# Kernel optimization log

Measured on AMD Instinct MI355X. Metric: run time of the kernel, lower is better.

The kernel has to match this reference:

```python
import jax, jax.numpy as jnp
import numpy as np


def setup_inputs() -> dict:
    key = jax.random.key(0)
    ks = jax.random.split(key, 7)
    B, C, H, W = 32, 512, 64, 64
    C8 = C // 8
    scale = 1.0 / np.sqrt(C)  # ~kaiming-ish for 1x1 conv
    return {
        "x": jax.random.normal(ks[0], (B, C, H, W), dtype=jnp.float32),
        "wq": jax.random.normal(ks[1], (C8, C), dtype=jnp.float32) * scale,
        "bq": jax.random.normal(ks[2], (C8,), dtype=jnp.float32) * 0.01,
        "wk": jax.random.normal(ks[3], (C8, C), dtype=jnp.float32) * scale,
        "bk": jax.random.normal(ks[4], (C8,), dtype=jnp.float32) * 0.01,
        "wv": jax.random.normal(ks[5], (C8, C), dtype=jnp.float32) * scale,
        "bv": jax.random.normal(ks[6], (C8,), dtype=jnp.float32) * 0.01,
    }


def reference(x, wq, bq, wk, bk, wv, bv):
    B, C, H, W = x.shape
    N = H * W
    xf = x.reshape(B, C, N)  # [B, C, N]
    # 1x1 convs == per-pixel linear projections C -> C//8
    q = jnp.einsum("bcn,oc->bon", xf, wq) + bq[None, :, None]  # [B, C8, N]
    k = jnp.einsum("bcn,oc->bon", xf, wk) + bk[None, :, None]  # [B, C8, N]
    v = jnp.einsum("bcn,oc->bon", xf, wv) + bv[None, :, None]  # [B, C8, N]
    # attention over channel pairs: [B, C8, C8], softmax over dim=-2 (rows)
    logits = jnp.einsum("bon,bpn->bop", q, k)
    attn = jax.nn.softmax(logits, axis=-2)
    out = jnp.einsum("bop,bpn->bon", attn, v)  # [B, C8, N]
    return out.mean(axis=-1)  # [B, C8]
```

## Files before the change

kernel.cpp:

```cpp
#include <hip/hip_runtime.h>


typedef __attribute__((ext_vector_type(8))) short short8;
typedef __attribute__((ext_vector_type(4))) float floatx4;
typedef __attribute__((ext_vector_type(4))) unsigned short ushort4v;

#define MFMA16(a, b, c) __builtin_amdgcn_mfma_f32_16x16x32_bf16((a), (b), (c), 0, 0, 0)

__device__ __forceinline__ unsigned short f2bf(float f) {
  unsigned int u = __float_as_uint(f);
  u = u + 0x7fffu + ((u >> 16) & 1u);
  return (unsigned short)(u >> 16);
}
__device__ __forceinline__ float bf2f(unsigned short h) {
  return __uint_as_float(((unsigned int)h) << 16);
}

constexpr int CB = 32;
constexpr int CC = 512;
constexpr int CO = 64;
constexpr int NN = 4096;
constexpr int NT = 128;
constexpr int KC = 32;
constexpr int NCH = CC / KC;

constexpr int XROW = 40;
constexpr int QROW = 72;

constexpr int WQH = 0;
constexpr int WQL = 2560;
constexpr int WKH = 5120;
constexpr int WKL = 7680;
constexpr int XHI = 10240;
constexpr int XLO = 15360;
constexpr int SMEM_U = 20480;
constexpr int QHI = 0, QLO = 4608, KHI = 9216, KLO = 13824;

__global__ __launch_bounds__(256, 2) void proj_kernel(
    const float* __restrict__ x, const float* __restrict__ wq,
    const float* __restrict__ bq, const float* __restrict__ wk,
    const float* __restrict__ bk, float* __restrict__ logits,
    float* __restrict__ xsum)
{
  __shared__ __align__(16) unsigned short smem[SMEM_U];

  const int t    = threadIdx.x;
  const int lane = t & 63;
  const int wave = t >> 6;
  const int quad = lane >> 4;
  const int l15  = lane & 15;
  const int b    = blockIdx.x >> 5;
  const int tile = blockIdx.x & 31;
  const int n0   = tile * NT;
  const int nlow = t & 31;
  const int chi  = t >> 5;

  floatx4 accq[4][2], acck[4][2];
#pragma unroll
  for (int mf = 0; mf < 4; ++mf)
#pragma unroll
    for (int nf = 0; nf < 2; ++nf) {
      accq[mf][nf] = (floatx4)0.0f;
      acck[mf][nf] = (floatx4)0.0f;
    }

  const float* xb = x + (size_t)b * CC * NN + n0;

  for (int ch = 0; ch < NCH; ++ch) {
    const int c0 = ch * KC;
    __syncthreads();

    float xs_part[4] = {0.f, 0.f, 0.f, 0.f};
#pragma unroll
    for (int i = 0; i < 4; ++i) {
      const int n = i * 32 + nlow;
      float v0 = xb[(size_t)(c0 + chi * 4 + 0) * NN + n];
      float v1 = xb[(size_t)(c0 + chi * 4 + 1) * NN + n];
      float v2 = xb[(size_t)(c0 + chi * 4 + 2) * NN + n];
      float v3 = xb[(size_t)(c0 + chi * 4 + 3) * NN + n];
      xs_part[0] += v0; xs_part[1] += v1; xs_part[2] += v2; xs_part[3] += v3;
      ushort4v h, l;
      h[0] = f2bf(v0); l[0] = f2bf(v0 - bf2f(h[0]));
      h[1] = f2bf(v1); l[1] = f2bf(v1 - bf2f(h[1]));
      h[2] = f2bf(v2); l[2] = f2bf(v2 - bf2f(h[2]));
      h[3] = f2bf(v3); l[3] = f2bf(v3 - bf2f(h[3]));
      *reinterpret_cast<ushort4v*>(&smem[XHI + n * XROW + chi * 4]) = h;
      *reinterpret_cast<ushort4v*>(&smem[XLO + n * XROW + chi * 4]) = l;
    }
#pragma unroll
    for (int j = 0; j < 4; ++j) {
      float v = xs_part[j];
      v += __shfl_xor(v, 16); v += __shfl_xor(v, 8);
      v += __shfl_xor(v, 4);  v += __shfl_xor(v, 2); v += __shfl_xor(v, 1);
      if ((lane & 31) == 0) atomicAdd(&xsum[b * CC + c0 + chi * 4 + j], v);
    }

#pragma unroll
    for (int i = 0; i < 2; ++i) {
      const int idx = t + i * 256;
      const int row = idx >> 3, cf = idx & 7;
      const floatx4 aq = *reinterpret_cast<const floatx4*>(
          &wq[(size_t)row * CC + c0 + cf * 4]);
      const floatx4 ak = *reinterpret_cast<const floatx4*>(
          &wk[(size_t)row * CC + c0 + cf * 4]);
      ushort4v qh, ql, kh, kl;
#pragma unroll
      for (int j = 0; j < 4; ++j) {
        qh[j] = f2bf(aq[j]); ql[j] = f2bf(aq[j] - bf2f(qh[j]));
        kh[j] = f2bf(ak[j]); kl[j] = f2bf(ak[j] - bf2f(kh[j]));
      }
      *reinterpret_cast<ushort4v*>(&smem[WQH + row * XROW + cf * 4]) = qh;
      *reinterpret_cast<ushort4v*>(&smem[WQL + row * XROW + cf * 4]) = ql;
      *reinterpret_cast<ushort4v*>(&smem[WKH + row * XROW + cf * 4]) = kh;
      *reinterpret_cast<ushort4v*>(&smem[WKL + row * XROW + cf * 4]) = kl;
    }
    __syncthreads();

    short8 xh[2], xl[2];
#pragma unroll
    for (int nf = 0; nf < 2; ++nf) {
      const int nr = wave * 32 + nf * 16 + l15;
      xh[nf] = *reinterpret_cast<const short8*>(&smem[XHI + nr * XROW + quad * 8]);
      xl[nf] = *reinterpret_cast<const short8*>(&smem[XLO + nr * XROW + quad * 8]);
    }
#pragma unroll
    for (int mf = 0; mf < 4; ++mf) {
      const int orow = mf * 16 + l15;
      const short8 aqh = *reinterpret_cast<const short8*>(&smem[WQH + orow * XROW + quad * 8]);
      const short8 aql = *reinterpret_cast<const short8*>(&smem[WQL + orow * XROW + quad * 8]);
      const short8 akh = *reinterpret_cast<const short8*>(&smem[WKH + orow * XROW + quad * 8]);
      const short8 akl = *reinterpret_cast<const short8*>(&smem[WKL + orow * XROW + quad * 8]);
#pragma unroll
      for (int nf = 0; nf < 2; ++nf) {
        accq[mf][nf] = MFMA16(aqh, xh[nf], accq[mf][nf]);
        accq[mf][nf] = MFMA16(aql, xh[nf], accq[mf][nf]);
        accq[mf][nf] = MFMA16(aqh, xl[nf], accq[mf][nf]);
        acck[mf][nf] = MFMA16(akh, xh[nf], acck[mf][nf]);
        acck[mf][nf] = MFMA16(akl, xh[nf], acck[mf][nf]);
        acck[mf][nf] = MFMA16(akh, xl[nf], acck[mf][nf]);
      }
    }
  }

#pragma unroll
  for (int mf = 0; mf < 4; ++mf)
#pragma unroll
    for (int r = 0; r < 4; ++r) {
      const int o = mf * 16 + quad * 4 + r;
      const float bqv = bq[o], bkv = bk[o];
#pragma unroll
      for (int nf = 0; nf < 2; ++nf) {
        accq[mf][nf][r] += bqv;
        acck[mf][nf][r] += bkv;
      }
    }

  floatx4 accS[4];
#pragma unroll
  for (int mf = 0; mf < 4; ++mf) accS[mf] = (floatx4)0.0f;

  for (int hh = 0; hh < 2; ++hh) {
    __syncthreads();
    if ((wave >> 1) == hh) {
      const int nbase = (wave & 1) * 32;
#pragma unroll
      for (int mf = 0; mf < 4; ++mf)
#pragma unroll
        for (int nf = 0; nf < 2; ++nf)
#pragma unroll
          for (int r = 0; r < 4; ++r) {
            const int o  = mf * 16 + quad * 4 + r;
            const int nc = nbase + nf * 16 + l15;
            const float qv = accq[mf][nf][r];
            const float kv = acck[mf][nf][r];
            const unsigned short qh = f2bf(qv);
            const unsigned short kh = f2bf(kv);
            smem[QHI + o * QROW + nc] = qh;
            smem[QLO + o * QROW + nc] = f2bf(qv - bf2f(qh));
            smem[KHI + o * QROW + nc] = kh;
            smem[KLO + o * QROW + nc] = f2bf(kv - bf2f(kh));
          }
    }
    __syncthreads();
#pragma unroll
    for (int ks = 0; ks < 2; ++ks) {
      const short8 bh = *reinterpret_cast<const short8*>(
          &smem[KHI + (wave * 16 + l15) * QROW + ks * 32 + quad * 8]);
      const short8 bl = *reinterpret_cast<const short8*>(
          &smem[KLO + (wave * 16 + l15) * QROW + ks * 32 + quad * 8]);
#pragma unroll
      for (int mf = 0; mf < 4; ++mf) {
        const short8 ah = *reinterpret_cast<const short8*>(
            &smem[QHI + (mf * 16 + l15) * QROW + ks * 32 + quad * 8]);
        const short8 al = *reinterpret_cast<const short8*>(
            &smem[QLO + (mf * 16 + l15) * QROW + ks * 32 + quad * 8]);
        accS[mf] = MFMA16(ah, bh, accS[mf]);
        accS[mf] = MFMA16(al, bh, accS[mf]);
        accS[mf] = MFMA16(ah, bl, accS[mf]);
      }
    }
  }

#pragma unroll
  for (int mf = 0; mf < 4; ++mf)
#pragma unroll
    for (int r = 0; r < 4; ++r) {
      const int o = mf * 16 + quad * 4 + r;
      const int p = wave * 16 + l15;
      atomicAdd(&logits[((size_t)b * CO + o) * CO + p], accS[mf][r]);
    }
}

__global__ __launch_bounds__(256) void zero_kernel(float* __restrict__ p, int n) {
  const int i = blockIdx.x * 256 + threadIdx.x;
  if (i < n) p[i] = 0.0f;
}

__global__ __launch_bounds__(256) void finalize_kernel(
    const float* __restrict__ wv, const float* __restrict__ bv,
    const float* __restrict__ logits, const float* __restrict__ xsum,
    float* __restrict__ out)
{
  __shared__ float ls[CO * 65];
  __shared__ float xs_s[CC];
  __shared__ float vbar_s[CO], w2_s[CO], cmax_s[CO];
  const int t = threadIdx.x;
  const int b = blockIdx.x;

  for (int i = t; i < CC; i += 256) xs_s[i] = xsum[b * CC + i];
#pragma unroll
  for (int i = 0; i < 16; ++i) {
    const int idx = t + i * 256;
    ls[(idx >> 6) * 65 + (idx & 63)] = logits[(size_t)b * CO * CO + idx];
  }
  __syncthreads();

  {
    const int p = t >> 2, part = t & 3;
    float s = 0.f;
    const float* wr = wv + (size_t)p * CC + part * 128;
    const float* xr = xs_s + part * 128;
#pragma unroll 4
    for (int c = 0; c < 128; ++c) s += wr[c] * xr[c];
    s += __shfl_xor(s, 1); s += __shfl_xor(s, 2);
    if (part == 0) vbar_s[p] = s * (1.0f / 4096.0f) + bv[p];
  }
  __syncthreads();

  if (t < CO) {
    float m = -1e30f;
    for (int o = 0; o < CO; ++o) m = fmaxf(m, ls[o * 65 + t]);
    float sum = 0.f;
    for (int o = 0; o < CO; ++o) sum += __expf(ls[o * 65 + t] - m);
    cmax_s[t] = m;
    w2_s[t]   = vbar_s[t] / sum;
  }
  __syncthreads();

  if (t < CO) {
    float acc = 0.f;
    for (int p = 0; p < CO; ++p)
      acc += __expf(ls[t * 65 + p] - cmax_s[p]) * w2_s[p];
    out[b * CO + t] = acc;
  }
}

extern "C" void kernel_launch(void* const* d_in, const int* in_sizes, int n_in,
                              void* d_out, int out_size, void* d_ws, size_t ws_size,
                              hipStream_t stream) {
  const float* x  = (const float*)d_in[0];
  const float* wq = (const float*)d_in[1];
  const float* bq = (const float*)d_in[2];
  const float* wk = (const float*)d_in[3];
  const float* bk = (const float*)d_in[4];
  const float* wv = (const float*)d_in[5];
  const float* bv = (const float*)d_in[6];
  float* out = (float*)d_out;

  float* logits = (float*)d_ws;
  float* xsum   = logits + CB * CO * CO;
  const int nzero = CB * CO * CO + CB * CC;

  zero_kernel<<<(nzero + 255) / 256, 256, 0, stream>>>(logits, nzero);
  proj_kernel<<<CB * (NN / NT), 256, 0, stream>>>(x, wq, bq, wk, bk, logits, xsum);
  finalize_kernel<<<CB, 256, 0, stream>>>(wv, bv, logits, xsum, out);
}
```

Baseline: 413.6 us.

## Preconvert weights to bf16 split layout and load x directly into MFMA registers

Adds a prep kernel that converts wq/wk/wv to hi/lo bf16 once, stored in an MFMA-friendly chunked layout in the workspace. The projection kernel now loads x straight from global memory into registers, double-buffered across channel chunks, and reads the weights from global/L2. This drops the per-chunk shared-memory staging and both __syncthreads. The v projection is also folded in as an extra bf16 MFMA with a per-block reduction into vsum, which replaces the xsum atomics and the wv matvec in finalize. The trade-offs are more register pressure, strided scalar global loads of x, and lower v precision (hi part only).

```diff
diff --git a/kernel.cpp b/kernel.cpp
--- a/kernel.cpp
+++ b/kernel.cpp
@@ -3,7 +3,6 @@
 
 typedef __attribute__((ext_vector_type(8))) short short8;
 typedef __attribute__((ext_vector_type(4))) float floatx4;
-typedef __attribute__((ext_vector_type(4))) unsigned short ushort4v;
 
 #define MFMA16(a, b, c) __builtin_amdgcn_mfma_f32_16x16x32_bf16((a), (b), (c), 0, 0, 0)
 
@@ -20,29 +19,43 @@
 constexpr int CC = 512;
 constexpr int CO = 64;
 constexpr int NN = 4096;
-constexpr int NT = 128;
-constexpr int KC = 32;
-constexpr int NCH = CC / KC;
-
-constexpr int XROW = 40;
 constexpr int QROW = 72;
 
-constexpr int WQH = 0;
-constexpr int WQL = 2560;
-constexpr int WKH = 5120;
-constexpr int WKL = 7680;
-constexpr int XHI = 10240;
-constexpr int XLO = 15360;
-constexpr int SMEM_U = 20480;
-constexpr int QHI = 0, QLO = 4608, KHI = 9216, KLO = 13824;
+constexpr int ZERO_CNT = CB * CO * CO + CB * CO;
+constexpr int WMAT  = 16 * 64 * 32;
+
+__global__ __launch_bounds__(256) void zero_kernel(float* __restrict__ p, int n) {
+  const int i = blockIdx.x * 256 + threadIdx.x;
+  if (i < n) p[i] = 0.0f;
+}
+
+__global__ __launch_bounds__(256) void prep_w_kernel(
+    const float* __restrict__ wq, const float* __restrict__ wk,
+    const float* __restrict__ wv, unsigned short* __restrict__ ws5)
+{
+  const int gid = blockIdx.x * 256 + threadIdx.x;
+#pragma unroll
+  for (int e = 0; e < 2; ++e) {
+    const int idx = e * 16384 + gid;
+    const int o = idx >> 9, c = idx & 511;
+    const int dst = ((c >> 5) * 64 + o) * 32 + (c & 31);
+    const float q = wq[idx], k = wk[idx], v = wv[idx];
+    const unsigned short qh = f2bf(q), kh = f2bf(k);
+    ws5[dst]             = qh;
+    ws5[dst + WMAT]      = f2bf(q - bf2f(qh));
+    ws5[dst + 2 * WMAT]  = kh;
+    ws5[dst + 3 * WMAT]  = f2bf(k - bf2f(kh));
+    ws5[dst + 4 * WMAT]  = f2bf(v);
+  }
+}
 
 __global__ __launch_bounds__(256, 2) void proj_kernel(
-    const float* __restrict__ x, const float* __restrict__ wq,
-    const float* __restrict__ bq, const float* __restrict__ wk,
-    const float* __restrict__ bk, float* __restrict__ logits,
-    float* __restrict__ xsum)
+    const float* __restrict__ x, const unsigned short* __restrict__ ws5,
+    const float* __restrict__ bq, const float* __restrict__ bk,
+    float* __restrict__ logits, float* __restrict__ vsum)
 {
-  __shared__ __align__(16) unsigned short smem[SMEM_U];
+  __shared__ __align__(16) unsigned short smem[4 * 64 * QROW];
+  __shared__ float vps[4][64];
 
   const int t    = threadIdx.x;
   const int lane = t & 63;
@@ -51,85 +64,47 @@
   const int l15  = lane & 15;
   const int b    = blockIdx.x >> 5;
   const int tile = blockIdx.x & 31;
-  const int n0   = tile * NT;
-  const int nlow = t & 31;
-  const int chi  = t >> 5;
-
-  floatx4 accq[4][2], acck[4][2];
+
+  floatx4 accq[4][2], acck[4][2], accv[4][2];
 #pragma unroll
   for (int mf = 0; mf < 4; ++mf)
 #pragma unroll
     for (int nf = 0; nf < 2; ++nf) {
       accq[mf][nf] = (floatx4)0.0f;
       acck[mf][nf] = (floatx4)0.0f;
-    }
-
-  const float* xb = x + (size_t)b * CC * NN + n0;
-
-  for (int ch = 0; ch < NCH; ++ch) {
-    const int c0 = ch * KC;
-    __syncthreads();
-
-    float xs_part[4] = {0.f, 0.f, 0.f, 0.f};
-#pragma unroll
-    for (int i = 0; i < 4; ++i) {
-      const int n = i * 32 + nlow;
-      float v0 = xb[(size_t)(c0 + chi * 4 + 0) * NN + n];
-      float v1 = xb[(size_t)(c0 + chi * 4 + 1) * NN + n];
-      float v2 = xb[(size_t)(c0 + chi * 4 + 2) * NN + n];
-      float v3 = xb[(size_t)(c0 + chi * 4 + 3) * NN + n];
-      xs_part[0] += v0; xs_part[1] += v1; xs_part[2] += v2; xs_part[3] += v3;
-      ushort4v h, l;
-      h[0] = f2bf(v0); l[0] = f2bf(v0 - bf2f(h[0]));
-      h[1] = f2bf(v1); l[1] = f2bf(v1 - bf2f(h[1]));
-      h[2] = f2bf(v2); l[2] = f2bf(v2 - bf2f(h[2]));
-      h[3] = f2bf(v3); l[3] = f2bf(v3 - bf2f(h[3]));
-      *reinterpret_cast<ushort4v*>(&smem[XHI + n * XROW + chi * 4]) = h;
-      *reinterpret_cast<ushort4v*>(&smem[XLO + n * XROW + chi * 4]) = l;
-    }
-#pragma unroll
-    for (int j = 0; j < 4; ++j) {
-      float v = xs_part[j];
-      v += __shfl_xor(v, 16); v += __shfl_xor(v, 8);
-      v += __shfl_xor(v, 4);  v += __shfl_xor(v, 2); v += __shfl_xor(v, 1);
-      if ((lane & 31) == 0) atomicAdd(&xsum[b * CC + c0 + chi * 4 + j], v);
-    }
-
-#pragma unroll
-    for (int i = 0; i < 2; ++i) {
-      const int idx = t + i * 256;
-      const int row = idx >> 3, cf = idx & 7;
-      const floatx4 aq = *reinterpret_cast<const floatx4*>(
-          &wq[(size_t)row * CC + c0 + cf * 4]);
-      const floatx4 ak = *reinterpret_cast<const floatx4*>(
-          &wk[(size_t)row * CC + c0 + cf * 4]);
-      ushort4v qh, ql, kh, kl;
-#pragma unroll
-      for (int j = 0; j < 4; ++j) {
-        qh[j] = f2bf(aq[j]); ql[j] = f2bf(aq[j] - bf2f(qh[j]));
-        kh[j] = f2bf(ak[j]); kl[j] = f2bf(ak[j] - bf2f(kh[j]));
-      }
-      *reinterpret_cast<ushort4v*>(&smem[WQH + row * XROW + cf * 4]) = qh;
-      *reinterpret_cast<ushort4v*>(&smem[WQL + row * XROW + cf * 4]) = ql;
-      *reinterpret_cast<ushort4v*>(&smem[WKH + row * XROW + cf * 4]) = kh;
-      *reinterpret_cast<ushort4v*>(&smem[WKL + row * XROW + cf * 4]) = kl;
-    }
-    __syncthreads();
-
+      accv[mf][nf] = (floatx4)0.0f;
+    }
+
+  const float* xp = x + (size_t)b * CC * NN + (size_t)(quad * 8) * NN
+                      + tile * 128 + wave * 32 + l15;
+
+  auto load_x = [&](float xv[2][8], const float* p) {
+#pragma unroll
+    for (int j = 0; j < 8; ++j) {
+      xv[0][j] = p[(size_t)j * NN];
+      xv[1][j] = p[(size_t)j * NN + 16];
+    }
+  };
+
+  auto compute = [&](const float xv[2][8], int ch) {
     short8 xh[2], xl[2];
 #pragma unroll
-    for (int nf = 0; nf < 2; ++nf) {
-      const int nr = wave * 32 + nf * 16 + l15;
-      xh[nf] = *reinterpret_cast<const short8*>(&smem[XHI + nr * XROW + quad * 8]);
-      xl[nf] = *reinterpret_cast<const short8*>(&smem[XLO + nr * XROW + quad * 8]);
-    }
+    for (int nf = 0; nf < 2; ++nf)
+#pragma unroll
+      for (int j = 0; j < 8; ++j) {
+        const unsigned short h = f2bf(xv[nf][j]);
+        xh[nf][j] = (short)h;
+        xl[nf][j] = (short)f2bf(xv[nf][j] - bf2f(h));
+      }
+    const unsigned short* wch = ws5 + ch * 2048 + l15 * 32 + quad * 8;
 #pragma unroll
     for (int mf = 0; mf < 4; ++mf) {
-      const int orow = mf * 16 + l15;
-      const short8 aqh = *reinterpret_cast<const short8*>(&smem[WQH + orow * XROW + quad * 8]);
-      const short8 aql = *reinterpret_cast<const short8*>(&smem[WQL + orow * XROW + quad * 8]);
-      const short8 akh = *reinterpret_cast<const short8*>(&smem[WKH + orow * XROW + quad * 8]);
-      const short8 akl = *reinterpret_cast<const short8*>(&smem[WKL + orow * XROW + quad * 8]);
+      const unsigned short* wo = wch + mf * 512;
+      const short8 aqh = *reinterpret_cast<const short8*>(wo);
+      const short8 aql = *reinterpret_cast<const short8*>(wo + WMAT);
+      const short8 akh = *reinterpret_cast<const short8*>(wo + 2 * WMAT);
+      const short8 akl = *reinterpret_cast<const short8*>(wo + 3 * WMAT);
+      const short8 avh = *reinterpret_cast<const short8*>(wo + 4 * WMAT);
 #pragma unroll
       for (int nf = 0; nf < 2; ++nf) {
         accq[mf][nf] = MFMA16(aqh, xh[nf], accq[mf][nf]);
@@ -138,9 +113,22 @@
         acck[mf][nf] = MFMA16(akh, xh[nf], acck[mf][nf]);
         acck[mf][nf] = MFMA16(akl, xh[nf], acck[mf][nf]);
         acck[mf][nf] = MFMA16(akh, xl[nf], acck[mf][nf]);
-      }
-    }
-  }
+        accv[mf][nf] = MFMA16(avh, xh[nf], accv[mf][nf]);
+      }
+    }
+  };
+
+  float xv0[2][8], xv1[2][8];
+  load_x(xv0, xp); xp += (size_t)32 * NN;
+  for (int ch = 0; ch < 14; ch += 2) {
+    load_x(xv1, xp); xp += (size_t)32 * NN;
+    compute(xv0, ch);
+    load_x(xv0, xp); xp += (size_t)32 * NN;
+    compute(xv1, ch + 1);
+  }
+  load_x(xv1, xp);
+  compute(xv0, 14);
+  compute(xv1, 15);
 
 #pragma unroll
   for (int mf = 0; mf < 4; ++mf)
@@ -155,6 +143,7 @@
       }
     }
 
+  constexpr int QHI = 0, QLO = 4608, KHI = 9216, KLO = 13824;
   floatx4 accS[4];
 #pragma unroll
   for (int mf = 0; mf < 4; ++mf) accS[mf] = (floatx4)0.0f;
@@ -209,41 +198,36 @@
       const int p = wave * 16 + l15;
       atomicAdd(&logits[((size_t)b * CO + o) * CO + p], accS[mf][r]);
     }
-}
-
-__global__ __launch_bounds__(256) void zero_kernel(float* __restrict__ p, int n) {
-  const int i = blockIdx.x * 256 + threadIdx.x;
-  if (i < n) p[i] = 0.0f;
+
+#pragma unroll
+  for (int mf = 0; mf < 4; ++mf)
+#pragma unroll
+    for (int r = 0; r < 4; ++r) {
+      float sv = accv[mf][0][r] + accv[mf][1][r];
+      sv += __shfl_xor(sv, 1); sv += __shfl_xor(sv, 2);
+      sv += __shfl_xor(sv, 4); sv += __shfl_xor(sv, 8);
+      if (l15 == 0) vps[wave][mf * 16 + quad * 4 + r] = sv;
+    }
+  __syncthreads();
+  if (t < CO) {
+    const float s = vps[0][t] + vps[1][t] + vps[2][t] + vps[3][t];
+    atomicAdd(&vsum[b * CO + t], s);
+  }
 }
 
 __global__ __launch_bounds__(256) void finalize_kernel(
-    const float* __restrict__ wv, const float* __restrict__ bv,
-    const float* __restrict__ logits, const float* __restrict__ xsum,
-    float* __restrict__ out)
+    const float* __restrict__ bv, const float* __restrict__ logits,
+    const float* __restrict__ vsum, float* __restrict__ out)
 {
   __shared__ float ls[CO * 65];
-  __shared__ float xs_s[CC];
-  __shared__ float vbar_s[CO], w2_s[CO], cmax_s[CO];
+  __shared__ float w2_s[CO], cmax_s[CO];
   const int t = threadIdx.x;
   const int b = blockIdx.x;
 
-  for (int i = t; i < CC; i += 256) xs_s[i] = xsum[b * CC + i];
 #pragma unroll
   for (int i = 0; i < 16; ++i) {
     const int idx = t + i * 256;
     ls[(idx >> 6) * 65 + (idx & 63)] = logits[(size_t)b * CO * CO + idx];
-  }
-  __syncthreads();
-
-  {
-    const int p = t >> 2, part = t & 3;
-    float s = 0.f;
-    const float* wr = wv + (size_t)p * CC + part * 128;
-    const float* xr = xs_s + part * 128;
-#pragma unroll 4
-    for (int c = 0; c < 128; ++c) s += wr[c] * xr[c];
-    s += __shfl_xor(s, 1); s += __shfl_xor(s, 2);
-    if (part == 0) vbar_s[p] = s * (1.0f / 4096.0f) + bv[p];
   }
   __syncthreads();
 
@@ -253,7 +237,8 @@
     float sum = 0.f;
     for (int o = 0; o < CO; ++o) sum += __expf(ls[o * 65 + t] - m);
     cmax_s[t] = m;
-    w2_s[t]   = vbar_s[t] / sum;
+    const float vbar = vsum[b * CO + t] * (1.0f / 4096.0f) + bv[t];
+    w2_s[t] = vbar / sum;
   }
   __syncthreads();
 
@@ -278,10 +263,11 @@
   float* out = (float*)d_out;
 
   float* logits = (float*)d_ws;
-  float* xsum   = logits + CB * CO * CO;
-  const int nzero = CB * CO * CO + CB * CC;
-
-  zero_kernel<<<(nzero + 255) / 256, 256, 0, stream>>>(logits, nzero);
-  proj_kernel<<<CB * (NN / NT), 256, 0, stream>>>(x, wq, bq, wk, bk, logits, xsum);
-  finalize_kernel<<<CB, 256, 0, stream>>>(wv, bv, logits, xsum, out);
-}
+  float* vsum   = logits + CB * CO * CO;
+  unsigned short* ws5 = (unsigned short*)(vsum + CB * CO);
+
+  zero_kernel<<<(ZERO_CNT + 255) / 256, 256, 0, stream>>>(logits, ZERO_CNT);
+  prep_w_kernel<<<64, 256, 0, stream>>>(wq, wk, wv, ws5);
+  proj_kernel<<<CB * 32, 256, 0, stream>>>(x, ws5, bq, bk, logits, vsum);
+  finalize_kernel<<<CB, 256, 0, stream>>>(bv, logits, vsum, out);
+}
```

New measurement: 414.2 us. About the same (+0.1%).
